# Kernel optimization log

Hardware: AMD Instinct MI355X
Metric: run time of the kernel (lower is better)

The kernel has to match this reference:

```python
import jax, jax.numpy as jnp
import numpy as np

E, H, I, T = 8, 1024, 2816, 8192  # experts, hidden, intermediate, total tokens


def setup_inputs() -> dict:
    key = jax.random.key(0)
    k1, k2, k3, k4 = jax.random.split(key, 4)
    x = jax.random.normal(k1, (T, H), dtype=jnp.float32)
    # xavier_normal std = sqrt(2 / (fan_in + fan_out))
    std = (2.0 / (H + I)) ** 0.5
    gate = jax.random.normal(k2, (E, H, I), dtype=jnp.float32) * std
    up = jax.random.normal(k3, (E, H, I), dtype=jnp.float32) * std
    down = jax.random.normal(k4, (E, I, H), dtype=jnp.float32) * std
    # tokens are pre-permuted so each expert's tokens are contiguous; equal split here
    tokens_per_expert = jnp.full((E,), T // E, dtype=jnp.int32)
    return {
        "permuted_local_hidden_states": x,
        "grouped_gate_proj": gate,
        "grouped_up_proj": up,
        "grouped_down_proj": down,
        "tokens_per_expert": tokens_per_expert,
    }


def reference(permuted_local_hidden_states, grouped_gate_proj, grouped_up_proj,
              grouped_down_proj, tokens_per_expert):
    # grouped GEMM: for expert e, rows in its contiguous segment are multiplied by W[e]
    o1 = jax.lax.ragged_dot(permuted_local_hidden_states, grouped_gate_proj,
                            tokens_per_expert)            # [T, I]
    o2 = jax.lax.ragged_dot(permuted_local_hidden_states, grouped_up_proj,
                            tokens_per_expert)            # [T, I]
    inter = jax.nn.silu(o1) * o2                          # SwiGLU  [T, I]
    out = jax.lax.ragged_dot(inter, grouped_down_proj, tokens_per_expert)  # [T, H]
    return out
```

## Files before the change

kernel.cpp:

```cpp
#include <hip/hip_runtime.h>
#include <hip/hip_bf16.h>


#define E_ 8
#define H_ 1024
#define I_ 2816
#define T_ 8192

typedef unsigned short u16;
typedef __attribute__((ext_vector_type(8))) short s16x8;
typedef __attribute__((ext_vector_type(8))) unsigned short u16x8;
typedef __attribute__((ext_vector_type(4))) float f32x4;

__device__ __forceinline__ void async16(const u16* g, u16* l) {
  __builtin_amdgcn_global_load_lds((__attribute__((address_space(1))) void*)g,
                                   (__attribute__((address_space(3))) void*)l, 16, 0, 0);
}

__device__ __forceinline__ u16 f2b(float f) {
  union { __hip_bfloat16 h; u16 u; } c;
  c.h = __float2bfloat16(f);
  return c.u;
}

__global__ __launch_bounds__(256) void convx_k(const float* __restrict__ x,
                                               u16* __restrict__ xb) {
  size_t i = ((size_t)blockIdx.x * 256 + threadIdx.x) * 8;
  float4 v0 = *(const float4*)(x + i);
  float4 v1 = *(const float4*)(x + i + 4);
  u16x8 b;
  b[0] = f2b(v0.x); b[1] = f2b(v0.y); b[2] = f2b(v0.z); b[3] = f2b(v0.w);
  b[4] = f2b(v1.x); b[5] = f2b(v1.y); b[6] = f2b(v1.z); b[7] = f2b(v1.w);
  *(u16x8*)(xb + i) = b;
}

template <int R, int C>
__device__ __forceinline__ void tconv_tile(const float* __restrict__ in,
                                           u16* __restrict__ out,
                                           int bx, int by, int t) {
  __shared__ float tile[64 * 64];
  const int c0 = bx * 64, r0 = by * 64;
  {
    const int rr = t >> 4;
    const int c4 = (t & 15) * 4;
#pragma unroll
    for (int j = 0; j < 4; ++j) {
      const int r = rr + 16 * j;
      float4 v = *(const float4*)(in + (size_t)(r0 + r) * C + c0 + c4);
      tile[r * 64 + ((c4 + 0) ^ r)] = v.x;
      tile[r * 64 + ((c4 + 1) ^ r)] = v.y;
      tile[r * 64 + ((c4 + 2) ^ r)] = v.z;
      tile[r * 64 + ((c4 + 3) ^ r)] = v.w;
    }
  }
  __syncthreads();
  {
    const int c = t >> 2;
    const int rq = (t & 3) * 8;
    u16* o = out + (size_t)(c0 + c) * R + r0;
    u16x8 b;
#pragma unroll
    for (int j = 0; j < 8; ++j) {
      const int r = rq + j;
      b[j] = f2b(tile[r * 64 + (c ^ r)]);
    }
    *(u16x8*)(o + rq) = b;
#pragma unroll
    for (int j = 0; j < 8; ++j) {
      const int r = 32 + rq + j;
      b[j] = f2b(tile[r * 64 + (c ^ r)]);
    }
    *(u16x8*)(o + 32 + rq) = b;
  }
}

__global__ __launch_bounds__(256) void tconvGU_k(const float* __restrict__ G,
                                                 const float* __restrict__ U,
                                                 u16* __restrict__ GT,
                                                 u16* __restrict__ UT) {
  const int z = blockIdx.z;
  const size_t eoff = (size_t)(z >> 1) * (size_t)H_ * I_;
  const float* in = ((z & 1) ? U : G) + eoff;
  u16* out = ((z & 1) ? UT : GT) + eoff;
  tconv_tile<H_, I_>(in, out, blockIdx.x, blockIdx.y, threadIdx.x);
}

__global__ __launch_bounds__(256) void tconvD_k(const float* __restrict__ D,
                                                u16* __restrict__ DT) {
  const size_t eoff = (size_t)blockIdx.z * (size_t)H_ * I_;
  tconv_tile<I_, H_>(D + eoff, DT + eoff, blockIdx.x, blockIdx.y, threadIdx.x);
}

__global__ __launch_bounds__(256, 2) void gemm12_k(
    const u16* __restrict__ X, const u16* __restrict__ GT,
    const u16* __restrict__ UT, const int* __restrict__ tpe,
    u16* __restrict__ inter) {
  __shared__ u16 sA[128 * 64];
  __shared__ u16 sG[64 * 64];
  __shared__ u16 sU[64 * 64];
  const int t = threadIdx.x;
  const int m0 = blockIdx.y * 128;
  const int n0 = blockIdx.x * 64;

  int e = 0, seg_end = T_;
  {
    int s = 0;
    for (int i = 0; i < E_; ++i) {
      int c = tpe[i];
      if (m0 < s + c) { e = i; seg_end = s + c; break; }
      s += c;
    }
  }
  const u16* GTe = GT + (size_t)e * I_ * H_;
  const u16* UTe = UT + (size_t)e * I_ * H_;

  const int sj = ((t & 7) ^ ((t >> 3) & 7)) * 8;
  const u16* gA = X + (size_t)(m0 + (t >> 3)) * H_ + sj;
  const u16* gG = GTe + (size_t)(n0 + (t >> 3)) * H_ + sj;
  const u16* gU = UTe + (size_t)(n0 + (t >> 3)) * H_ + sj;
  u16* lA = sA + t * 8;
  u16* lG = sG + t * 8;
  u16* lU = sU + t * 8;

  const int l = t & 63, w = t >> 6;
  const int wm = (w & 1) * 64, wn = (w >> 1) * 32;
  const int c0 = (((l >> 4) ^ (l & 7))) * 8;
  const u16* fA = sA + (size_t)(wm + (l & 15)) * 64;
  const u16* fG = sG + (size_t)(wn + (l & 15)) * 64;
  const u16* fU = sU + (size_t)(wn + (l & 15)) * 64;

  f32x4 accG[4][2], accU[4][2];
#pragma unroll
  for (int mi = 0; mi < 4; ++mi)
#pragma unroll
    for (int ni = 0; ni < 2; ++ni) {
      accG[mi][ni] = (f32x4){0.f, 0.f, 0.f, 0.f};
      accU[mi][ni] = (f32x4){0.f, 0.f, 0.f, 0.f};
    }

  for (int k0 = 0; k0 < H_; k0 += 64) {
    async16(gA + k0, lA);
    async16(gA + 32 * H_ + k0, lA + 2048);
    async16(gA + 64 * H_ + k0, lA + 4096);
    async16(gA + 96 * H_ + k0, lA + 6144);
    async16(gG + k0, lG);
    async16(gG + 32 * H_ + k0, lG + 2048);
    async16(gU + k0, lU);
    async16(gU + 32 * H_ + k0, lU + 2048);
    __syncthreads();
#pragma unroll
    for (int ks = 0; ks < 2; ++ks) {
      const int co = c0 ^ (ks * 32);
      s16x8 aF[4], gF[2], uF[2];
#pragma unroll
      for (int mi = 0; mi < 4; ++mi) aF[mi] = *(const s16x8*)(fA + mi * 1024 + co);
#pragma unroll
      for (int ni = 0; ni < 2; ++ni) {
        gF[ni] = *(const s16x8*)(fG + ni * 1024 + co);
        uF[ni] = *(const s16x8*)(fU + ni * 1024 + co);
      }
#pragma unroll
      for (int mi = 0; mi < 4; ++mi)
#pragma unroll
        for (int ni = 0; ni < 2; ++ni) {
          accG[mi][ni] = __builtin_amdgcn_mfma_f32_16x16x32_bf16(aF[mi], gF[ni], accG[mi][ni], 0, 0, 0);
          accU[mi][ni] = __builtin_amdgcn_mfma_f32_16x16x32_bf16(aF[mi], uF[ni], accU[mi][ni], 0, 0, 0);
        }
    }
    __syncthreads();
  }

  const int colb = l & 15, rowb = (l >> 4) * 4;
#pragma unroll
  for (int mi = 0; mi < 4; ++mi)
#pragma unroll
    for (int ni = 0; ni < 2; ++ni) {
      const size_t gcol = (size_t)(n0 + wn + ni * 16 + colb);
#pragma unroll
      for (int r = 0; r < 4; ++r) {
        int grow = m0 + wm + mi * 16 + rowb + r;
        if (grow < seg_end) {
          float o1 = accG[mi][ni][r];
          float o2 = accU[mi][ni][r];
          float sv = o1 / (1.f + __expf(-o1));
          inter[(size_t)grow * I_ + gcol] = f2b(sv * o2);
        }
      }
    }
}

__global__ __launch_bounds__(256, 2) void gemm3_k(
    const u16* __restrict__ A, const u16* __restrict__ DT,
    const int* __restrict__ tpe, float* __restrict__ out,
    float* __restrict__ part) {
  __shared__ u16 sA[128 * 64];
  __shared__ u16 sB[128 * 64];
  const int t = threadIdx.x;
  const int m0 = blockIdx.y * 128;
  const int n0 = blockIdx.x * 128;
  const int ks = blockIdx.z;
  const int kbase = ks * (I_ / 2);

  int e = 0, seg_end = T_;
  {
    int s = 0;
    for (int i = 0; i < E_; ++i) {
      int c = tpe[i];
      if (m0 < s + c) { e = i; seg_end = s + c; break; }
      s += c;
    }
  }
  const u16* DTe = DT + (size_t)e * H_ * I_;

  const int sj = ((t & 7) ^ ((t >> 3) & 7)) * 8;
  const u16* gA = A + (size_t)(m0 + (t >> 3)) * I_ + kbase + sj;
  const u16* gB = DTe + (size_t)(n0 + (t >> 3)) * I_ + kbase + sj;
  u16* lA = sA + t * 8;
  u16* lB = sB + t * 8;

  const int l = t & 63, w = t >> 6;
  const int wm = (w & 1) * 64, wn = (w >> 1) * 64;
  const int c0 = (((l >> 4) ^ (l & 7))) * 8;
  const u16* fA = sA + (size_t)(wm + (l & 15)) * 64;
  const u16* fB = sB + (size_t)(wn + (l & 15)) * 64;

  f32x4 acc[4][4];
#pragma unroll
  for (int mi = 0; mi < 4; ++mi)
#pragma unroll
    for (int ni = 0; ni < 4; ++ni) acc[mi][ni] = (f32x4){0.f, 0.f, 0.f, 0.f};

  for (int k0 = 0; k0 < I_ / 2; k0 += 64) {
    async16(gA + k0, lA);
    async16(gA + 32 * I_ + k0, lA + 2048);
    async16(gA + 64 * I_ + k0, lA + 4096);
    async16(gA + 96 * I_ + k0, lA + 6144);
    async16(gB + k0, lB);
    async16(gB + 32 * I_ + k0, lB + 2048);
    async16(gB + 64 * I_ + k0, lB + 4096);
    async16(gB + 96 * I_ + k0, lB + 6144);
    __syncthreads();
#pragma unroll
    for (int kk = 0; kk < 2; ++kk) {
      const int co = c0 ^ (kk * 32);
      s16x8 aF[4], bF[4];
#pragma unroll
      for (int mi = 0; mi < 4; ++mi) aF[mi] = *(const s16x8*)(fA + mi * 1024 + co);
#pragma unroll
      for (int ni = 0; ni < 4; ++ni) bF[ni] = *(const s16x8*)(fB + ni * 1024 + co);
#pragma unroll
      for (int mi = 0; mi < 4; ++mi)
#pragma unroll
        for (int ni = 0; ni < 4; ++ni)
          acc[mi][ni] = __builtin_amdgcn_mfma_f32_16x16x32_bf16(aF[mi], bF[ni], acc[mi][ni], 0, 0, 0);
    }
    __syncthreads();
  }

  float* dst = ks ? part : out;
  const int colb = l & 15, rowb = (l >> 4) * 4;
#pragma unroll
  for (int mi = 0; mi < 4; ++mi)
#pragma unroll
    for (int ni = 0; ni < 4; ++ni) {
      const size_t gcol = (size_t)(n0 + wn + ni * 16 + colb);
#pragma unroll
      for (int r = 0; r < 4; ++r) {
        int grow = m0 + wm + mi * 16 + rowb + r;
        if (grow < seg_end) dst[(size_t)grow * H_ + gcol] = acc[mi][ni][r];
      }
    }
}

__global__ __launch_bounds__(256) void add_k(float* __restrict__ out,
                                             const float* __restrict__ part) {
  size_t i = ((size_t)blockIdx.x * 256 + threadIdx.x) * 8;
  float4 a0 = *(float4*)(out + i);
  float4 a1 = *(float4*)(out + i + 4);
  float4 b0 = *(const float4*)(part + i);
  float4 b1 = *(const float4*)(part + i + 4);
  a0.x += b0.x; a0.y += b0.y; a0.z += b0.z; a0.w += b0.w;
  a1.x += b1.x; a1.y += b1.y; a1.z += b1.z; a1.w += b1.w;
  *(float4*)(out + i) = a0;
  *(float4*)(out + i + 4) = a1;
}

extern "C" void kernel_launch(void* const* d_in, const int* in_sizes, int n_in,
                              void* d_out, int out_size, void* d_ws, size_t ws_size,
                              hipStream_t stream) {
  const float* X = (const float*)d_in[0];
  const float* G = (const float*)d_in[1];
  const float* U = (const float*)d_in[2];
  const float* D = (const float*)d_in[3];
  const int* tpe = (const int*)d_in[4];
  float* out = (float*)d_out;

  const size_t W = (size_t)E_ * H_ * I_;
  if (ws_size < 3 * W * sizeof(u16)) return;
  u16* r0 = (u16*)d_ws;
  u16* r1 = r0 + W;
  u16* r2 = r1 + W;
  u16* xb = (u16*)d_out;
  float* part = (float*)r1;

  convx_k<<<dim3((T_ * H_) / (256 * 8)), 256, 0, stream>>>(X, xb);
  tconvGU_k<<<dim3(I_ / 64, H_ / 64, E_ * 2), 256, 0, stream>>>(G, U, r0, r1);
  gemm12_k<<<dim3(I_ / 64, T_ / 128), 256, 0, stream>>>(xb, r0, r1, tpe, r2);
  tconvD_k<<<dim3(H_ / 64, I_ / 64, E_), 256, 0, stream>>>(D, r0);
  gemm3_k<<<dim3(H_ / 128, T_ / 128, 2), 256, 0, stream>>>(r2, r0, tpe, out, part);
  add_k<<<dim3((T_ * H_) / (256 * 8)), 256, 0, stream>>>(out, part);
}
```

Before: 486.6 us.

## Drop split-K in down GEMM with narrower tiles; transpose weights without LDS

The down-projection GEMM no longer splits K across two blocks with a partial buffer and a separate add kernel. Each block now covers a 128x64 output tile over the full K range, so the grid has the same block count without the extra partial write, read and kernel launch. The weight transpose-convert kernels also drop the shared-memory tile and read strided columns straight from global memory. That transpose change skips a barrier and LDS traffic but loses coalescing on the fp32 reads, since each thread now walks down rows.

Result: faster. 477.1 us (-2.0%).

```diff
diff --git a/kernel.cpp b/kernel.cpp
--- a/kernel.cpp
+++ b/kernel.cpp
@@ -38,40 +38,18 @@
 __device__ __forceinline__ void tconv_tile(const float* __restrict__ in,
                                            u16* __restrict__ out,
                                            int bx, int by, int t) {
-  __shared__ float tile[64 * 64];
   const int c0 = bx * 64, r0 = by * 64;
-  {
-    const int rr = t >> 4;
-    const int c4 = (t & 15) * 4;
-#pragma unroll
-    for (int j = 0; j < 4; ++j) {
-      const int r = rr + 16 * j;
-      float4 v = *(const float4*)(in + (size_t)(r0 + r) * C + c0 + c4);
-      tile[r * 64 + ((c4 + 0) ^ r)] = v.x;
-      tile[r * 64 + ((c4 + 1) ^ r)] = v.y;
-      tile[r * 64 + ((c4 + 2) ^ r)] = v.z;
-      tile[r * 64 + ((c4 + 3) ^ r)] = v.w;
-    }
-  }
-  __syncthreads();
-  {
-    const int c = t >> 2;
-    const int rq = (t & 3) * 8;
-    u16* o = out + (size_t)(c0 + c) * R + r0;
-    u16x8 b;
-#pragma unroll
-    for (int j = 0; j < 8; ++j) {
-      const int r = rq + j;
-      b[j] = f2b(tile[r * 64 + (c ^ r)]);
-    }
-    *(u16x8*)(o + rq) = b;
-#pragma unroll
-    for (int j = 0; j < 8; ++j) {
-      const int r = 32 + rq + j;
-      b[j] = f2b(tile[r * 64 + (c ^ r)]);
-    }
-    *(u16x8*)(o + 32 + rq) = b;
-  }
+  const int c = c0 + (t >> 2);
+  const int rq = (t & 3) * 8;
+  const float* p = in + (size_t)r0 * C + c;
+  u16* o = out + (size_t)c * R + r0;
+  u16x8 b;
+#pragma unroll
+  for (int j = 0; j < 8; ++j) b[j] = f2b(p[(size_t)(rq + j) * C]);
+  *(u16x8*)(o + rq) = b;
+#pragma unroll
+  for (int j = 0; j < 8; ++j) b[j] = f2b(p[(size_t)(32 + rq + j) * C]);
+  *(u16x8*)(o + 32 + rq) = b;
 }
 
 __global__ __launch_bounds__(256) void tconvGU_k(const float* __restrict__ G,
@@ -191,15 +169,12 @@
 
 __global__ __launch_bounds__(256, 2) void gemm3_k(
     const u16* __restrict__ A, const u16* __restrict__ DT,
-    const int* __restrict__ tpe, float* __restrict__ out,
-    float* __restrict__ part) {
+    const int* __restrict__ tpe, float* __restrict__ out) {
   __shared__ u16 sA[128 * 64];
-  __shared__ u16 sB[128 * 64];
+  __shared__ u16 sB[64 * 64];
   const int t = threadIdx.x;
   const int m0 = blockIdx.y * 128;
-  const int n0 = blockIdx.x * 128;
-  const int ks = blockIdx.z;
-  const int kbase = ks * (I_ / 2);
+  const int n0 = blockIdx.x * 64;
 
   int e = 0, seg_end = T_;
   {
@@ -213,76 +188,60 @@
   const u16* DTe = DT + (size_t)e * H_ * I_;
 
   const int sj = ((t & 7) ^ ((t >> 3) & 7)) * 8;
-  const u16* gA = A + (size_t)(m0 + (t >> 3)) * I_ + kbase + sj;
-  const u16* gB = DTe + (size_t)(n0 + (t >> 3)) * I_ + kbase + sj;
+  const u16* gA = A + (size_t)(m0 + (t >> 3)) * I_ + sj;
+  const u16* gB = DTe + (size_t)(n0 + (t >> 3)) * I_ + sj;
   u16* lA = sA + t * 8;
   u16* lB = sB + t * 8;
 
   const int l = t & 63, w = t >> 6;
-  const int wm = (w & 1) * 64, wn = (w >> 1) * 64;
+  const int wm = (w & 1) * 64, wn = (w >> 1) * 32;
   const int c0 = (((l >> 4) ^ (l & 7))) * 8;
   const u16* fA = sA + (size_t)(wm + (l & 15)) * 64;
   const u16* fB = sB + (size_t)(wn + (l & 15)) * 64;
 
-  f32x4 acc[4][4];
-#pragma unroll
-  for (int mi = 0; mi < 4; ++mi)
-#pragma unroll
-    for (int ni = 0; ni < 4; ++ni) acc[mi][ni] = (f32x4){0.f, 0.f, 0.f, 0.f};
-
-  for (int k0 = 0; k0 < I_ / 2; k0 += 64) {
+  f32x4 acc[4][2];
+#pragma unroll
+  for (int mi = 0; mi < 4; ++mi)
+#pragma unroll
+    for (int ni = 0; ni < 2; ++ni) acc[mi][ni] = (f32x4){0.f, 0.f, 0.f, 0.f};
+
+  for (int k0 = 0; k0 < I_; k0 += 64) {
     async16(gA + k0, lA);
     async16(gA + 32 * I_ + k0, lA + 2048);
     async16(gA + 64 * I_ + k0, lA + 4096);
     async16(gA + 96 * I_ + k0, lA + 6144);
     async16(gB + k0, lB);
     async16(gB + 32 * I_ + k0, lB + 2048);
-    async16(gB + 64 * I_ + k0, lB + 4096);
-    async16(gB + 96 * I_ + k0, lB + 6144);
-    __syncthreads();
-#pragma unroll
-    for (int kk = 0; kk < 2; ++kk) {
-      const int co = c0 ^ (kk * 32);
-      s16x8 aF[4], bF[4];
+    __syncthreads();
+#pragma unroll
+    for (int ks = 0; ks < 2; ++ks) {
+      const int co = c0 ^ (ks * 32);
+      s16x8 aF[4], bF[2];
 #pragma unroll
       for (int mi = 0; mi < 4; ++mi) aF[mi] = *(const s16x8*)(fA + mi * 1024 + co);
 #pragma unroll
-      for (int ni = 0; ni < 4; ++ni) bF[ni] = *(const s16x8*)(fB + ni * 1024 + co);
+      for (int ni = 0; ni < 2; ++ni) bF[ni] = *(const s16x8*)(fB + ni * 1024 + co);
 #pragma unroll
       for (int mi = 0; mi < 4; ++mi)
 #pragma unroll
-        for (int ni = 0; ni < 4; ++ni)
+        for (int ni = 0; ni < 2; ++ni)
           acc[mi][ni] = __builtin_amdgcn_mfma_f32_16x16x32_bf16(aF[mi], bF[ni], acc[mi][ni], 0, 0, 0);
     }
     __syncthreads();
   }
 
-  float* dst = ks ? part : out;
   const int colb = l & 15, rowb = (l >> 4) * 4;
 #pragma unroll
   for (int mi = 0; mi < 4; ++mi)
 #pragma unroll
-    for (int ni = 0; ni < 4; ++ni) {
+    for (int ni = 0; ni < 2; ++ni) {
       const size_t gcol = (size_t)(n0 + wn + ni * 16 + colb);
 #pragma unroll
       for (int r = 0; r < 4; ++r) {
         int grow = m0 + wm + mi * 16 + rowb + r;
-        if (grow < seg_end) dst[(size_t)grow * H_ + gcol] = acc[mi][ni][r];
+        if (grow < seg_end) out[(size_t)grow * H_ + gcol] = acc[mi][ni][r];
       }
     }
-}
-
-__global__ __launch_bounds__(256) void add_k(float* __restrict__ out,
-                                             const float* __restrict__ part) {
-  size_t i = ((size_t)blockIdx.x * 256 + threadIdx.x) * 8;
-  float4 a0 = *(float4*)(out + i);
-  float4 a1 = *(float4*)(out + i + 4);
-  float4 b0 = *(const float4*)(part + i);
-  float4 b1 = *(const float4*)(part + i + 4);
-  a0.x += b0.x; a0.y += b0.y; a0.z += b0.z; a0.w += b0.w;
-  a1.x += b1.x; a1.y += b1.y; a1.z += b1.z; a1.w += b1.w;
-  *(float4*)(out + i) = a0;
-  *(float4*)(out + i + 4) = a1;
 }
 
 extern "C" void kernel_launch(void* const* d_in, const int* in_sizes, int n_in,
@@ -301,12 +260,10 @@
   u16* r1 = r0 + W;
   u16* r2 = r1 + W;
   u16* xb = (u16*)d_out;
-  float* part = (float*)r1;
 
   convx_k<<<dim3((T_ * H_) / (256 * 8)), 256, 0, stream>>>(X, xb);
   tconvGU_k<<<dim3(I_ / 64, H_ / 64, E_ * 2), 256, 0, stream>>>(G, U, r0, r1);
   gemm12_k<<<dim3(I_ / 64, T_ / 128), 256, 0, stream>>>(xb, r0, r1, tpe, r2);
   tconvD_k<<<dim3(H_ / 64, I_ / 64, E_), 256, 0, stream>>>(D, r0);
-  gemm3_k<<<dim3(H_ / 128, T_ / 128, 2), 256, 0, stream>>>(r2, r0, tpe, out, part);
-  add_k<<<dim3((T_ * H_) / (256 * 8)), 256, 0, stream>>>(out, part);
-}
+  gemm3_k<<<dim3(H_ / 64, T_ / 128), 256, 0, stream>>>(r2, r0, tpe, out);
+}
```
